# Kernel optimization log

Measured on AMD Instinct MI355X. Metric: run time of the kernel, lower is better.

Reference implementation:

```python
import jax, jax.numpy as jnp
from jax import lax
import numpy as np

B, N, F_IN, H, K, F_OUT = 8, 4096, 40, 64, 5, 1


def setup_inputs() -> dict:
    key = jax.random.key(0)
    ks = jax.random.split(key, 10)
    x = jax.random.normal(ks[0], (B, N, F_IN), dtype=jnp.float32)
    adjacency_matrix = jax.random.uniform(ks[1], (N, N), dtype=jnp.float32)
    s1 = 1.0 / np.sqrt(F_IN)
    s2 = 1.0 / np.sqrt(H)
    W1 = jax.random.uniform(ks[2], (F_IN, H), minval=-s1, maxval=s1, dtype=jnp.float32)
    b1 = jax.random.uniform(ks[3], (H,), minval=-s1, maxval=s1, dtype=jnp.float32)
    W2 = jax.random.uniform(ks[4], (H, H), minval=-s2, maxval=s2, dtype=jnp.float32)
    b2 = jax.random.uniform(ks[5], (H,), minval=-s2, maxval=s2, dtype=jnp.float32)
    sc = 1.0 / np.sqrt(H * K)
    conv_w = jax.random.uniform(ks[6], (H, H, K), minval=-sc, maxval=sc, dtype=jnp.float32)
    conv_b = jax.random.uniform(ks[7], (H,), minval=-sc, maxval=sc, dtype=jnp.float32)
    fc_w = jax.random.uniform(ks[8], (H, F_OUT), minval=-s2, maxval=s2, dtype=jnp.float32)
    fc_b = jax.random.uniform(ks[9], (F_OUT,), minval=-s2, maxval=s2, dtype=jnp.float32)
    return {"x": x, "adjacency_matrix": adjacency_matrix, "W1": W1, "b1": b1,
            "W2": W2, "b2": b2, "conv_w": conv_w, "conv_b": conv_b,
            "fc_w": fc_w, "fc_b": fc_b}


def reference(x, adjacency_matrix, W1, b1, W2, b2, conv_w, conv_b, fc_w, fc_b):
    # GraphConvolution 1: A @ (x @ W1) + b1  -> [B, N, H]
    h = jnp.einsum('nm,bmh->bnh', adjacency_matrix, x @ W1) + b1
    # GraphConvolution 2: A @ (h @ W2) + b2  -> [B, N, H]
    h = jnp.einsum('nm,bmh->bnh', adjacency_matrix, h @ W2) + b2
    # Temporal Conv1d over node/time axis: channels-first [B, H, N]
    h = jnp.transpose(h, (0, 2, 1))
    h = lax.conv_general_dilated(h, conv_w, window_strides=(1,), padding='VALID',
                                 dimension_numbers=('NCH', 'OIH', 'NCH'))
    h = h + conv_b[None, :, None]  # [B, H, N-K+1]
    h = jnp.mean(h, axis=2)        # mean over length (torch dim=2)
    return h @ fc_w + fc_b         # [B, 1]
```

## Files before the change

kernel.cpp:

```cpp
#include <hip/hip_runtime.h>

#define NN 4096
#define COL4 (NN / 4)
#define BB 8
#define F_IN 40
#define HH 64
#define KW 5
#define LL (NN - KW + 1)
#define RC 32
#define CHUNK (NN / RC)
#define PC 16
#define PCH (NN / PC)
#define PCH4 (PCH / 4)

#define OFF_P1 0
#define OFF_PE (OFF_P1 + RC * NN)
#define OFF_PD (OFF_PE + RC * 8 * NN)
#define OFF_XP (OFF_PD + RC * NN)
#define OFF_BW (OFF_XP + 64 * 9 * 64)
#define OFF_M  (OFF_BW + 64)
#define OFF_AB (OFF_M + 9 * F_IN)
#define OFF_G9 (OFF_AB + 9)
#define OFF_RP (OFF_G9 + 9)
#define OFF_SC (OFF_RP + 8 * 16)
#define OFF_SP (OFF_SC + 32)

__device__ __forceinline__ int special_row(int s) { return s < 4 ? s : (NN - 8 + s); }
__device__ __forceinline__ void f4add(float4& a, const float4& b) {
    a.x += b.x; a.y += b.y; a.z += b.z; a.w += b.w;
}
__device__ __forceinline__ void f4fma(float4& a, float w, const float4& b) {
    a.x += w * b.x; a.y += w * b.y; a.z += w * b.z; a.w += w * b.w;
}

__global__ __launch_bounds__(256) void kA(const float4* __restrict__ A4,
                                          const float* __restrict__ A,
                                          float4* __restrict__ part1,
                                          float4* __restrict__ partE,
                                          float* __restrict__ rpart,
                                          const float* __restrict__ b1,
                                          const float* __restrict__ W2,
                                          const float* __restrict__ cw,
                                          const float* __restrict__ fw,
                                          float* __restrict__ Xpart,
                                          float* __restrict__ bw2) {
    int tx = threadIdx.x, ty = threadIdx.y;
    int tid = ty * 64 + tx;
    if (blockIdx.x < 512) {
        __shared__ float w[8][CHUNK];
        __shared__ float4 red3[4][3][64];
        int bx = blockIdx.x & 15, by = blockIdx.x >> 4;
        int m0 = by * CHUNK;
        for (int idx = tid; idx < 8 * CHUNK; idx += 256) {
            int s = idx >> 7, j = idx & 127;
            w[s][j] = A[(size_t)special_row(s) * NN + m0 + j];
        }
        __syncthreads();
        int c4 = bx * 64 + tx;
        const float4* Ap = A4 + (size_t)(m0 + ty * 32) * COL4 + c4;
        float4 acc[9];
        #pragma unroll
        for (int v = 0; v < 9; ++v) acc[v] = make_float4(0.f, 0.f, 0.f, 0.f);
        #pragma unroll 4
        for (int j = 0; j < 32; ++j) {
            float4 a = Ap[(size_t)j * COL4];
            int jj = ty * 32 + j;
            f4add(acc[0], a);
            #pragma unroll
            for (int s = 0; s < 8; ++s) f4fma(acc[1 + s], w[s][jj], a);
        }
        #pragma unroll
        for (int g = 0; g < 3; ++g) {
            #pragma unroll
            for (int vv = 0; vv < 3; ++vv) red3[ty][vv][tx] = acc[g * 3 + vv];
            __syncthreads();
            if (ty == 0) {
                #pragma unroll
                for (int vv = 0; vv < 3; ++vv) {
                    int v = g * 3 + vv;
                    float4 t = red3[0][vv][tx];
                    f4add(t, red3[1][vv][tx]);
                    f4add(t, red3[2][vv][tx]);
                    f4add(t, red3[3][vv][tx]);
                    if (v == 0) part1[(size_t)by * COL4 + c4] = t;
                    else        partE[((size_t)by * 8 + (v - 1)) * COL4 + c4] = t;
                }
            }
            __syncthreads();
        }
        if ((by == 0 || by == 31) && ty == 0) {
            int sbase = (by == 0) ? 0 : 4;
            #pragma unroll
            for (int k = 0; k < 4; ++k) {
                float4 a = A4[(size_t)special_row(sbase + k) * COL4 + c4];
                float v = a.x + a.y + a.z + a.w;
                for (int off = 32; off > 0; off >>= 1) v += __shfl_down(v, off);
                if (tx == 0) rpart[(sbase + k) * 16 + bx] = v;
            }
        }
        return;
    }
    if (blockIdx.x < 576) {
        int o = blockIdx.x - 512;
        if (tid < 64) {
            int i = tid;
            float f = fw[o];
            const float* cwp = cw + ((size_t)o * HH + i) * KW;
            float w0 = cwp[0], w1 = cwp[1], w2 = cwp[2], w3 = cwp[3], w4 = cwp[4];
            float* xp = Xpart + (size_t)o * 576 + i;
            xp[0]       = f * (w0 + w1 + w2 + w3 + w4);
            xp[64]      = f * (w1 + w2 + w3 + w4);
            xp[128]     = f * (w2 + w3 + w4);
            xp[192]     = f * (w3 + w4);
            xp[256]     = f * w4;
            xp[320]     = f * w0;
            xp[384]     = f * (w0 + w1);
            xp[448]     = f * (w0 + w1 + w2);
            xp[512]     = f * (w0 + w1 + w2 + w3);
        }
        return;
    }
    {
        __shared__ float W2s[64 * 65];
        __shared__ float b1s[64];
        for (int idx = tid; idx < 64 * 64; idx += 256)
            W2s[(idx >> 6) * 65 + (idx & 63)] = W2[idx];
        if (tid < 64) b1s[tid] = b1[tid];
        __syncthreads();
        if (tid < 64) {
            float s = 0.f;
            #pragma unroll 8
            for (int h = 0; h < 64; ++h) s += b1s[h] * W2s[h * 65 + tid];
            bw2[tid] = s;
        }
    }
}

__global__ __launch_bounds__(256) void kC(const float4* __restrict__ A4,
                                          const float* __restrict__ part1f,
                                          float4* __restrict__ partD,
                                          float* __restrict__ sCpart,
                                          const float* __restrict__ Xpart,
                                          const float* __restrict__ bw2,
                                          const float* __restrict__ W1,
                                          const float* __restrict__ W2,
                                          const float* __restrict__ b2,
                                          const float* __restrict__ cb,
                                          const float* __restrict__ fw,
                                          const float* __restrict__ fb,
                                          float* __restrict__ Mout,
                                          float* __restrict__ AB,
                                          float* __restrict__ G9) {
    int tid = threadIdx.x;
    if (blockIdx.x < 512) {
        int bx = blockIdx.x & 15, by = blockIdx.x >> 4;
        int tx = tid & 63, ty = tid >> 6;
        __shared__ float cs[CHUNK];
        __shared__ float4 redd[4][64];
        int m0 = by * CHUNK;
        if (tid < CHUNK) {
            float s = 0.f;
            #pragma unroll 8
            for (int y = 0; y < RC; ++y) s += part1f[(size_t)y * NN + m0 + tid];
            cs[tid] = s;
        }
        __syncthreads();
        if (bx == 0 && tid < 64) {
            float t = cs[tid] + cs[tid + 64];
            for (int off = 32; off > 0; off >>= 1) t += __shfl_down(t, off);
            if (tid == 0) sCpart[by] = t;
        }
        int c4 = bx * 64 + tx;
        const float4* Ap = A4 + (size_t)(m0 + ty * 32) * COL4 + c4;
        float4 acc = {0.f, 0.f, 0.f, 0.f};
        #pragma unroll 8
        for (int j = 0; j < 32; ++j) f4fma(acc, cs[ty * 32 + j], Ap[(size_t)j * COL4]);
        redd[ty][tx] = acc;
        __syncthreads();
        if (ty == 0) {
            float4 t = redd[0][tx];
            f4add(t, redd[1][tx]);
            f4add(t, redd[2][tx]);
            f4add(t, redd[3][tx]);
            partD[(size_t)by * COL4 + c4] = t;
        }
        return;
    }
    int v = blockIdx.x - 512;
    __shared__ float W2s[64 * 65];
    __shared__ float W1s[40 * 65];
    __shared__ float Xs[64];
    __shared__ float Ps[64];
    __shared__ float bw2s[64];
    __shared__ float b2s[64];
    __shared__ float fcb_s;
    for (int idx = tid; idx < 64 * 64; idx += 256)
        W2s[(idx >> 6) * 65 + (idx & 63)] = W2[idx];
    for (int idx = tid; idx < 40 * 64; idx += 256)
        W1s[(idx >> 6) * 65 + (idx & 63)] = W1[idx];
    if (tid < 64) { bw2s[tid] = bw2[tid]; b2s[tid] = b2[tid]; }
    if (tid == 0) fcb_s = 0.f;
    __syncthreads();
    if (tid < 64) {
        float s = 0.f;
        #pragma unroll 8
        for (int o = 0; o < 64; ++o) s += Xpart[(size_t)o * 576 + v * 64 + tid];
        Xs[tid] = (v == 0 ? 1.f : -1.f) * s / (float)LL;
    }
    __syncthreads();
    if (tid < 64) {
        float s = 0.f;
        #pragma unroll 8
        for (int i = 0; i < 64; ++i) s += Xs[i] * W2s[tid * 65 + i];
        Ps[tid] = s;
    }
    __syncthreads();
    if (tid < F_IN) {
        float s = 0.f;
        #pragma unroll 8
        for (int h = 0; h < 64; ++h) s += Ps[h] * W1s[tid * 65 + h];
        Mout[v * F_IN + tid] = s;
    }
    if (tid >= 64 && tid < 128) {
        int i = tid - 64;
        float a = Xs[i] * bw2s[i];
        for (int off = 32; off > 0; off >>= 1) a += __shfl_down(a, off);
        if (i == 0) AB[v] = a;
    }
    if (v == 0 && tid >= 128 && tid < 192) {
        int o = tid - 128;
        float t = fw[o] * cb[o];
        for (int off = 32; off > 0; off >>= 1) t += __shfl_down(t, off);
        if (o == 0) fcb_s = t;
    }
    __syncthreads();
    if (tid < 64) {
        float g = Xs[tid] * (v == 0 ? (float)NN * b2s[tid] : b2s[tid]);
        for (int off = 32; off > 0; off >>= 1) g += __shfl_down(g, off);
        if (tid == 0) G9[v] = g + (v == 0 ? fcb_s + fb[0] : 0.f);
    }
}

__global__ __launch_bounds__(256) void kE(const float* __restrict__ x,
                                          const float* __restrict__ partDf,
                                          const float* __restrict__ partEf,
                                          const float* __restrict__ M,
                                          float* __restrict__ spart) {
    __shared__ float xs[PCH * F_IN];
    __shared__ float wls[9][PCH];
    __shared__ float Ms[9 * F_IN];
    __shared__ float red[256];
    int b = blockIdx.x, pc = blockIdx.y;
    int tid = threadIdx.x;
    int p0 = pc * PCH;
    const float4* xsrc4 = (const float4*)(x + ((size_t)b * NN + p0) * F_IN);
    float4* xs4 = (float4*)xs;
    #pragma unroll 4
    for (int idx = tid; idx < PCH * F_IN / 4; idx += 256) xs4[idx] = xsrc4[idx];
    for (int idx = tid; idx < 9 * PCH4; idx += 256) {
        int v = idx / PCH4, j4 = idx % PCH4;
        float4 s = {0.f, 0.f, 0.f, 0.f};
        if (v == 0) {
            #pragma unroll 8
            for (int y = 0; y < RC; ++y)
                f4add(s, ((const float4*)partDf)[(size_t)y * COL4 + pc * PCH4 + j4]);
        } else {
            #pragma unroll 8
            for (int y = 0; y < RC; ++y)
                f4add(s, ((const float4*)partEf)[((size_t)y * 8 + (v - 1)) * COL4 + pc * PCH4 + j4]);
        }
        ((float4*)&wls[v][0])[j4] = s;
    }
    for (int idx = tid; idx < 9 * F_IN; idx += 256) Ms[idx] = M[idx];
    __syncthreads();
    float part = 0.f;
    for (int o = tid; o < 9 * F_IN; o += 256) {
        int v = o / F_IN, f = o % F_IN;
        float s = 0.f;
        for (int j = 0; j < PCH; ++j) s += wls[v][j] * xs[j * F_IN + f];
        part += Ms[o] * s;
    }
    red[tid] = part;
    __syncthreads();
    for (int off = 128; off > 0; off >>= 1) {
        if (tid < off) red[tid] += red[tid + off];
        __syncthreads();
    }
    if (tid == 0) spart[(size_t)b * PC + pc] = red[0];
}

__global__ void kF(const float* __restrict__ spart, const float* __restrict__ rpart,
                   const float* __restrict__ sCpart, const float* __restrict__ AB,
                   const float* __restrict__ G9, float* __restrict__ out) {
    int tid = threadIdx.x;
    __shared__ float red[128];
    __shared__ float c0s;
    float val = AB[1 + (tid >> 4)] * rpart[tid];
    if (tid < 32) val += AB[0] * sCpart[tid];
    if (tid < 9)  val += G9[tid];
    red[tid] = val;
    __syncthreads();
    for (int off = 64; off > 0; off >>= 1) {
        if (tid < off) red[tid] += red[tid + off];
        __syncthreads();
    }
    if (tid == 0) c0s = red[0];
    __syncthreads();
    float s = spart[tid];
    for (int off = 8; off > 0; off >>= 1) s += __shfl_down(s, off, 16);
    if ((tid & 15) == 0) out[tid >> 4] = c0s + s;
}

extern "C" void kernel_launch(void* const* d_in, const int* in_sizes, int n_in,
                              void* d_out, int out_size, void* d_ws, size_t ws_size,
                              hipStream_t stream) {
    const float* x  = (const float*)d_in[0];
    const float* A  = (const float*)d_in[1];
    const float* W1 = (const float*)d_in[2];
    const float* b1 = (const float*)d_in[3];
    const float* W2 = (const float*)d_in[4];
    const float* b2 = (const float*)d_in[5];
    const float* cw = (const float*)d_in[6];
    const float* cb = (const float*)d_in[7];
    const float* fw = (const float*)d_in[8];
    const float* fb = (const float*)d_in[9];
    float* out = (float*)d_out;
    float* ws = (float*)d_ws;

    float* part1 = ws + OFF_P1;
    float* partE = ws + OFF_PE;
    float* partD = ws + OFF_PD;
    float* Xpart = ws + OFF_XP;
    float* bw2   = ws + OFF_BW;
    float* Mmat  = ws + OFF_M;
    float* AB    = ws + OFF_AB;
    float* G9    = ws + OFF_G9;
    float* rpart = ws + OFF_RP;
    float* sCpart= ws + OFF_SC;
    float* spart = ws + OFF_SP;

    const float4* A4 = (const float4*)A;

    kA<<<dim3(577), dim3(64, 4), 0, stream>>>(A4, A, (float4*)part1, (float4*)partE, rpart,
                                              b1, W2, cw, fw, Xpart, bw2);
    kC<<<dim3(521), 256, 0, stream>>>(A4, part1, (float4*)partD, sCpart,
                                      Xpart, bw2, W1, W2, b2, cb, fw, fb, Mmat, AB, G9);
    kE<<<dim3(BB, PC), 256, 0, stream>>>(x, partD, partE, Mmat, spart);
    kF<<<dim3(1), 128, 0, stream>>>(spart, rpart, sCpart, AB, G9, out);
}
```

Baseline: 54.62 us.

## Drop final reduction kernel, fold constant term into kC and atomically accumulate in kE

Removes the single-block kF launch. kC now uses one block instead of nine to compute all nine M/AB/G9 vectors, folds them into the scalar constant and writes it to out. kE uses 512 blocks of 64 nodes instead of 128 blocks of 256 and atomically adds its partial sums into out. The column-sum total sCsum moves into kA via atomics, which adds a memset. The trade is one fewer launch and more parallel kE against float atomics that make the summation order nondeterministic.

```diff
diff --git a/kernel.cpp b/kernel.cpp
--- a/kernel.cpp
+++ b/kernel.cpp
@@ -9,21 +9,15 @@
 #define LL (NN - KW + 1)
 #define RC 32
 #define CHUNK (NN / RC)
-#define PC 16
-#define PCH (NN / PC)
-#define PCH4 (PCH / 4)
 
 #define OFF_P1 0
 #define OFF_PE (OFF_P1 + RC * NN)
 #define OFF_PD (OFF_PE + RC * 8 * NN)
 #define OFF_XP (OFF_PD + RC * NN)
-#define OFF_BW (OFF_XP + 64 * 9 * 64)
+#define OFF_BW (OFF_XP + 64 * 576)
 #define OFF_M  (OFF_BW + 64)
-#define OFF_AB (OFF_M + 9 * F_IN)
-#define OFF_G9 (OFF_AB + 9)
-#define OFF_RP (OFF_G9 + 9)
-#define OFF_SC (OFF_RP + 8 * 16)
-#define OFF_SP (OFF_SC + 32)
+#define OFF_RP (OFF_M + 9 * F_IN)
+#define OFF_SCS (OFF_RP + 128)
 
 __device__ __forceinline__ int special_row(int s) { return s < 4 ? s : (NN - 8 + s); }
 __device__ __forceinline__ void f4add(float4& a, const float4& b) {
@@ -38,6 +32,7 @@
                                           float4* __restrict__ part1,
                                           float4* __restrict__ partE,
                                           float* __restrict__ rpart,
+                                          float* __restrict__ sCsum,
                                           const float* __restrict__ b1,
                                           const float* __restrict__ W2,
                                           const float* __restrict__ cw,
@@ -47,16 +42,16 @@
     int tx = threadIdx.x, ty = threadIdx.y;
     int tid = ty * 64 + tx;
     if (blockIdx.x < 512) {
-        __shared__ float w[8][CHUNK];
+        __shared__ float wsh[8][CHUNK];
         __shared__ float4 red3[4][3][64];
-        int bx = blockIdx.x & 15, by = blockIdx.x >> 4;
-        int m0 = by * CHUNK;
+        const int bx = blockIdx.x & 15, by = blockIdx.x >> 4;
+        const int m0 = by * CHUNK;
         for (int idx = tid; idx < 8 * CHUNK; idx += 256) {
             int s = idx >> 7, j = idx & 127;
-            w[s][j] = A[(size_t)special_row(s) * NN + m0 + j];
-        }
-        __syncthreads();
-        int c4 = bx * 64 + tx;
+            wsh[s][j] = A[(size_t)special_row(s) * NN + m0 + j];
+        }
+        __syncthreads();
+        const int c4 = bx * 64 + tx;
         const float4* Ap = A4 + (size_t)(m0 + ty * 32) * COL4 + c4;
         float4 acc[9];
         #pragma unroll
@@ -67,7 +62,7 @@
             int jj = ty * 32 + j;
             f4add(acc[0], a);
             #pragma unroll
-            for (int s = 0; s < 8; ++s) f4fma(acc[1 + s], w[s][jj], a);
+            for (int s = 0; s < 8; ++s) f4fma(acc[1 + s], wsh[s][jj], a);
         }
         #pragma unroll
         for (int g = 0; g < 3; ++g) {
@@ -82,8 +77,14 @@
                     f4add(t, red3[1][vv][tx]);
                     f4add(t, red3[2][vv][tx]);
                     f4add(t, red3[3][vv][tx]);
-                    if (v == 0) part1[(size_t)by * COL4 + c4] = t;
-                    else        partE[((size_t)by * 8 + (v - 1)) * COL4 + c4] = t;
+                    if (v == 0) {
+                        part1[(size_t)by * COL4 + c4] = t;
+                        float val = t.x + t.y + t.z + t.w;
+                        for (int off = 32; off > 0; off >>= 1) val += __shfl_down(val, off);
+                        if (tx == 0) atomicAdd(sCsum, val);
+                    } else {
+                        partE[((size_t)by * 8 + (v - 1)) * COL4 + c4] = t;
+                    }
                 }
             }
             __syncthreads();
@@ -108,29 +109,26 @@
             const float* cwp = cw + ((size_t)o * HH + i) * KW;
             float w0 = cwp[0], w1 = cwp[1], w2 = cwp[2], w3 = cwp[3], w4 = cwp[4];
             float* xp = Xpart + (size_t)o * 576 + i;
-            xp[0]       = f * (w0 + w1 + w2 + w3 + w4);
-            xp[64]      = f * (w1 + w2 + w3 + w4);
-            xp[128]     = f * (w2 + w3 + w4);
-            xp[192]     = f * (w3 + w4);
-            xp[256]     = f * w4;
-            xp[320]     = f * w0;
-            xp[384]     = f * (w0 + w1);
-            xp[448]     = f * (w0 + w1 + w2);
-            xp[512]     = f * (w0 + w1 + w2 + w3);
+            xp[0]   = f * (w0 + w1 + w2 + w3 + w4);
+            xp[64]  = f * (w1 + w2 + w3 + w4);
+            xp[128] = f * (w2 + w3 + w4);
+            xp[192] = f * (w3 + w4);
+            xp[256] = f * w4;
+            xp[320] = f * w0;
+            xp[384] = f * (w0 + w1);
+            xp[448] = f * (w0 + w1 + w2);
+            xp[512] = f * (w0 + w1 + w2 + w3);
         }
         return;
     }
     {
-        __shared__ float W2s[64 * 65];
         __shared__ float b1s[64];
-        for (int idx = tid; idx < 64 * 64; idx += 256)
-            W2s[(idx >> 6) * 65 + (idx & 63)] = W2[idx];
         if (tid < 64) b1s[tid] = b1[tid];
         __syncthreads();
         if (tid < 64) {
             float s = 0.f;
             #pragma unroll 8
-            for (int h = 0; h < 64; ++h) s += b1s[h] * W2s[h * 65 + tid];
+            for (int h = 0; h < 64; ++h) s += b1s[h] * W2[h * HH + tid];
             bw2[tid] = s;
         }
     }
@@ -139,9 +137,10 @@
 __global__ __launch_bounds__(256) void kC(const float4* __restrict__ A4,
                                           const float* __restrict__ part1f,
                                           float4* __restrict__ partD,
-                                          float* __restrict__ sCpart,
                                           const float* __restrict__ Xpart,
-                                          const float* __restrict__ bw2,
+                                          const float* __restrict__ bw2g,
+                                          const float* __restrict__ rpart,
+                                          const float* __restrict__ sCsum,
                                           const float* __restrict__ W1,
                                           const float* __restrict__ W2,
                                           const float* __restrict__ b2,
@@ -149,15 +148,14 @@
                                           const float* __restrict__ fw,
                                           const float* __restrict__ fb,
                                           float* __restrict__ Mout,
-                                          float* __restrict__ AB,
-                                          float* __restrict__ G9) {
+                                          float* __restrict__ out) {
     int tid = threadIdx.x;
     if (blockIdx.x < 512) {
-        int bx = blockIdx.x & 15, by = blockIdx.x >> 4;
-        int tx = tid & 63, ty = tid >> 6;
+        const int bx = blockIdx.x & 15, by = blockIdx.x >> 4;
+        const int tx = tid & 63, ty = tid >> 6;
         __shared__ float cs[CHUNK];
         __shared__ float4 redd[4][64];
-        int m0 = by * CHUNK;
+        const int m0 = by * CHUNK;
         if (tid < CHUNK) {
             float s = 0.f;
             #pragma unroll 8
@@ -165,12 +163,7 @@
             cs[tid] = s;
         }
         __syncthreads();
-        if (bx == 0 && tid < 64) {
-            float t = cs[tid] + cs[tid + 64];
-            for (int off = 32; off > 0; off >>= 1) t += __shfl_down(t, off);
-            if (tid == 0) sCpart[by] = t;
-        }
-        int c4 = bx * 64 + tx;
+        const int c4 = bx * 64 + tx;
         const float4* Ap = A4 + (size_t)(m0 + ty * 32) * COL4 + c4;
         float4 acc = {0.f, 0.f, 0.f, 0.f};
         #pragma unroll 8
@@ -186,90 +179,111 @@
         }
         return;
     }
-    int v = blockIdx.x - 512;
     __shared__ float W2s[64 * 65];
     __shared__ float W1s[40 * 65];
-    __shared__ float Xs[64];
-    __shared__ float Ps[64];
+    __shared__ float Xs[9 * 64];
+    __shared__ float Ps[9 * 64];
     __shared__ float bw2s[64];
     __shared__ float b2s[64];
-    __shared__ float fcb_s;
+    __shared__ float ABs[9];
+    __shared__ float G9s[9];
+    __shared__ float fcb_s, c0s;
     for (int idx = tid; idx < 64 * 64; idx += 256)
         W2s[(idx >> 6) * 65 + (idx & 63)] = W2[idx];
     for (int idx = tid; idx < 40 * 64; idx += 256)
         W1s[(idx >> 6) * 65 + (idx & 63)] = W1[idx];
-    if (tid < 64) { bw2s[tid] = bw2[tid]; b2s[tid] = b2[tid]; }
-    if (tid == 0) fcb_s = 0.f;
-    __syncthreads();
-    if (tid < 64) {
+    if (tid < 64) { bw2s[tid] = bw2g[tid]; b2s[tid] = b2[tid]; }
+    __syncthreads();
+    for (int t = tid; t < 576; t += 256) {
+        int v = t >> 6, i = t & 63;
         float s = 0.f;
         #pragma unroll 8
-        for (int o = 0; o < 64; ++o) s += Xpart[(size_t)o * 576 + v * 64 + tid];
-        Xs[tid] = (v == 0 ? 1.f : -1.f) * s / (float)LL;
-    }
-    __syncthreads();
-    if (tid < 64) {
+        for (int o = 0; o < 64; ++o) s += Xpart[(size_t)o * 576 + v * 64 + i];
+        Xs[t] = (v == 0 ? 1.f : -1.f) * s / (float)LL;
+    }
+    __syncthreads();
+    for (int t = tid; t < 576; t += 256) {
+        int v = t >> 6, h = t & 63;
         float s = 0.f;
         #pragma unroll 8
-        for (int i = 0; i < 64; ++i) s += Xs[i] * W2s[tid * 65 + i];
-        Ps[tid] = s;
-    }
-    __syncthreads();
-    if (tid < F_IN) {
+        for (int i = 0; i < 64; ++i) s += Xs[v * 64 + i] * W2s[h * 65 + i];
+        Ps[t] = s;
+    }
+    __syncthreads();
+    for (int t = tid; t < 9 * F_IN; t += 256) {
+        int v = t / F_IN, f = t % F_IN;
         float s = 0.f;
         #pragma unroll 8
-        for (int h = 0; h < 64; ++h) s += Ps[h] * W1s[tid * 65 + h];
-        Mout[v * F_IN + tid] = s;
-    }
-    if (tid >= 64 && tid < 128) {
-        int i = tid - 64;
-        float a = Xs[i] * bw2s[i];
-        for (int off = 32; off > 0; off >>= 1) a += __shfl_down(a, off);
-        if (i == 0) AB[v] = a;
-    }
-    if (v == 0 && tid >= 128 && tid < 192) {
-        int o = tid - 128;
-        float t = fw[o] * cb[o];
-        for (int off = 32; off > 0; off >>= 1) t += __shfl_down(t, off);
-        if (o == 0) fcb_s = t;
-    }
-    __syncthreads();
-    if (tid < 64) {
-        float g = Xs[tid] * (v == 0 ? (float)NN * b2s[tid] : b2s[tid]);
-        for (int off = 32; off > 0; off >>= 1) g += __shfl_down(g, off);
-        if (tid == 0) G9[v] = g + (v == 0 ? fcb_s + fb[0] : 0.f);
-    }
+        for (int h = 0; h < 64; ++h) s += Ps[v * 64 + h] * W1s[f * 65 + h];
+        Mout[t] = s;
+    }
+    if (tid >= 192 && tid < 201) {
+        int v = tid - 192;
+        float a = 0.f;
+        #pragma unroll 8
+        for (int i = 0; i < 64; ++i) a += Xs[v * 64 + i] * bw2s[i];
+        ABs[v] = a;
+    }
+    if (tid >= 208 && tid < 217) {
+        int v = tid - 208;
+        float g = 0.f;
+        #pragma unroll 8
+        for (int i = 0; i < 64; ++i)
+            g += Xs[v * 64 + i] * (v == 0 ? (float)NN * b2s[i] : b2s[i]);
+        G9s[v] = g;
+    }
+    if (tid == 224) {
+        float t2 = 0.f;
+        #pragma unroll 8
+        for (int o = 0; o < 64; ++o) t2 += fw[o] * cb[o];
+        fcb_s = t2 + fb[0];
+    }
+    __syncthreads();
+    if (tid == 0) {
+        float c0 = fcb_s;
+        #pragma unroll
+        for (int v = 0; v < 9; ++v) c0 += G9s[v];
+        c0 += ABs[0] * sCsum[0];
+        #pragma unroll
+        for (int s = 0; s < 8; ++s) {
+            float r = 0.f;
+            #pragma unroll
+            for (int g = 0; g < 16; ++g) r += rpart[s * 16 + g];
+            c0 += ABs[1 + s] * r;
+        }
+        c0s = c0;
+    }
+    __syncthreads();
+    if (tid < BB) out[tid] = c0s;
 }
 
 __global__ __launch_bounds__(256) void kE(const float* __restrict__ x,
                                           const float* __restrict__ partDf,
                                           const float* __restrict__ partEf,
                                           const float* __restrict__ M,
-                                          float* __restrict__ spart) {
-    __shared__ float xs[PCH * F_IN];
-    __shared__ float wls[9][PCH];
+                                          float* __restrict__ out) {
+    __shared__ float xs[64 * F_IN];
+    __shared__ float wls[9 * 68];
     __shared__ float Ms[9 * F_IN];
     __shared__ float red[256];
-    int b = blockIdx.x, pc = blockIdx.y;
-    int tid = threadIdx.x;
-    int p0 = pc * PCH;
-    const float4* xsrc4 = (const float4*)(x + ((size_t)b * NN + p0) * F_IN);
+    const int b = blockIdx.x >> 6, pc = blockIdx.x & 63;
+    const int tid = threadIdx.x;
+    const float4* xsrc4 = (const float4*)(x + ((size_t)b * NN + pc * 64) * F_IN);
     float4* xs4 = (float4*)xs;
-    #pragma unroll 4
-    for (int idx = tid; idx < PCH * F_IN / 4; idx += 256) xs4[idx] = xsrc4[idx];
-    for (int idx = tid; idx < 9 * PCH4; idx += 256) {
-        int v = idx / PCH4, j4 = idx % PCH4;
+    for (int idx = tid; idx < 64 * F_IN / 4; idx += 256) xs4[idx] = xsrc4[idx];
+    for (int idx = tid; idx < 9 * 16; idx += 256) {
+        int v = idx >> 4, j4 = idx & 15;
         float4 s = {0.f, 0.f, 0.f, 0.f};
         if (v == 0) {
             #pragma unroll 8
             for (int y = 0; y < RC; ++y)
-                f4add(s, ((const float4*)partDf)[(size_t)y * COL4 + pc * PCH4 + j4]);
+                f4add(s, ((const float4*)partDf)[(size_t)y * COL4 + pc * 16 + j4]);
         } else {
             #pragma unroll 8
             for (int y = 0; y < RC; ++y)
-                f4add(s, ((const float4*)partEf)[((size_t)y * 8 + (v - 1)) * COL4 + pc * PCH4 + j4]);
-        }
-        ((float4*)&wls[v][0])[j4] = s;
+                f4add(s, ((const float4*)partEf)[((size_t)y * 8 + (v - 1)) * COL4 + pc * 16 + j4]);
+        }
+        *(float4*)&wls[v * 68 + j4 * 4] = s;
     }
     for (int idx = tid; idx < 9 * F_IN; idx += 256) Ms[idx] = M[idx];
     __syncthreads();
@@ -277,7 +291,8 @@
     for (int o = tid; o < 9 * F_IN; o += 256) {
         int v = o / F_IN, f = o % F_IN;
         float s = 0.f;
-        for (int j = 0; j < PCH; ++j) s += wls[v][j] * xs[j * F_IN + f];
+        #pragma unroll 8
+        for (int j = 0; j < 64; ++j) s += wls[v * 68 + j] * xs[j * F_IN + f];
         part += Ms[o] * s;
     }
     red[tid] = part;
@@ -286,29 +301,7 @@
         if (tid < off) red[tid] += red[tid + off];
         __syncthreads();
     }
-    if (tid == 0) spart[(size_t)b * PC + pc] = red[0];
-}
-
-__global__ void kF(const float* __restrict__ spart, const float* __restrict__ rpart,
-                   const float* __restrict__ sCpart, const float* __restrict__ AB,
-                   const float* __restrict__ G9, float* __restrict__ out) {
-    int tid = threadIdx.x;
-    __shared__ float red[128];
-    __shared__ float c0s;
-    float val = AB[1 + (tid >> 4)] * rpart[tid];
-    if (tid < 32) val += AB[0] * sCpart[tid];
-    if (tid < 9)  val += G9[tid];
-    red[tid] = val;
-    __syncthreads();
-    for (int off = 64; off > 0; off >>= 1) {
-        if (tid < off) red[tid] += red[tid + off];
-        __syncthreads();
-    }
-    if (tid == 0) c0s = red[0];
-    __syncthreads();
-    float s = spart[tid];
-    for (int off = 8; off > 0; off >>= 1) s += __shfl_down(s, off, 16);
-    if ((tid & 15) == 0) out[tid >> 4] = c0s + s;
+    if (tid == 0) atomicAdd(&out[b], red[0]);
 }
 
 extern "C" void kernel_launch(void* const* d_in, const int* in_sizes, int n_in,
@@ -325,7 +318,7 @@
     const float* fw = (const float*)d_in[8];
     const float* fb = (const float*)d_in[9];
     float* out = (float*)d_out;
-    float* ws = (float*)d_ws;
+    float* ws  = (float*)d_ws;
 
     float* part1 = ws + OFF_P1;
     float* partE = ws + OFF_PE;
@@ -333,18 +326,15 @@
     float* Xpart = ws + OFF_XP;
     float* bw2   = ws + OFF_BW;
     float* Mmat  = ws + OFF_M;
-    float* AB    = ws + OFF_AB;
-    float* G9    = ws + OFF_G9;
     float* rpart = ws + OFF_RP;
-    float* sCpart= ws + OFF_SC;
-    float* spart = ws + OFF_SP;
+    float* sCsum = ws + OFF_SCS;
 
     const float4* A4 = (const float4*)A;
 
-    kA<<<dim3(577), dim3(64, 4), 0, stream>>>(A4, A, (float4*)part1, (float4*)partE, rpart,
-                                              b1, W2, cw, fw, Xpart, bw2);
-    kC<<<dim3(521), 256, 0, stream>>>(A4, part1, (float4*)partD, sCpart,
-                                      Xpart, bw2, W1, W2, b2, cb, fw, fb, Mmat, AB, G9);
-    kE<<<dim3(BB, PC), 256, 0, stream>>>(x, partD, partE, Mmat, spart);
-    kF<<<dim3(1), 128, 0, stream>>>(spart, rpart, sCpart, AB, G9, out);
-}
+    hipMemsetAsync(sCsum, 0, sizeof(float), stream);
+    kA<<<dim3(577), dim3(64, 4), 0, stream>>>(A4, A, (float4*)part1, (float4*)partE,
+                                              rpart, sCsum, b1, W2, cw, fw, Xpart, bw2);
+    kC<<<dim3(513), 256, 0, stream>>>(A4, part1, (float4*)partD, Xpart, bw2, rpart, sCsum,
+                                      W1, W2, b2, cb, fw, fb, Mmat, out);
+    kE<<<dim3(512), 256, 0, stream>>>(x, partD, partE, Mmat, out);
+}
```

Result: slower. 72.16 us (+32.1%).
